# Performance work log

Measured on AMD Instinct MI355X. Metric: run time of the kernel, lower is better.

## Reference

```python
import jax, jax.numpy as jnp
import numpy as np

B, T, S, D, V, PAD = 8, 4095, 2048, 300, 32000, 1


def setup_inputs() -> dict:
    key = jax.random.key(0)
    k1, k2, k3, k4 = jax.random.split(key, 4)
    # tokens in [2, V) so none collide with padding_idx
    x = jax.random.randint(k1, (B, T), 2, V, dtype=jnp.int64)
    # first S nodes are leaves: indices (i, i); remaining T-S are internal spans hi > lo
    leaf = jnp.arange(S, dtype=jnp.int64)
    leaf_pairs = jnp.broadcast_to(jnp.stack([leaf, leaf], -1)[None], (B, S, 2))
    n_int = T - S
    lo = jax.random.randint(k2, (B, n_int), 0, S - 1, dtype=jnp.int64)
    span = jax.random.randint(k3, (B, n_int), 1, 64, dtype=jnp.int64)
    hi = jnp.minimum(lo + span, S - 1)
    int_pairs = jnp.stack([lo, hi], -1)
    indices = jnp.concatenate([leaf_pairs, int_pairs], axis=1)  # [B, T, 2]
    W = jax.random.normal(k4, (V, D), jnp.float32) * 0.02
    W = W.at[PAD].set(0.0)  # padding_idx row is zero, as in nn.Embedding
    return {"x": x, "indices": indices, "W": W}


def reference(x, indices, W):
    b, t = x.shape
    s = (t + 1) // 2
    # _retrieve_leaves: left-pack tokens whose (lo==hi) and token != PAD
    is_leaf = (indices[:, :, 0] == indices[:, :, 1]) & (x != PAD)  # [b,t]
    pos = jnp.cumsum(is_leaf.astype(jnp.int32), axis=1) - 1       # packed slot per leaf
    safe_pos = jnp.where(is_leaf, pos, s)                          # out-of-range -> dropped
    leaves = jnp.full((b, s), PAD, dtype=x.dtype)
    leaves = leaves.at[jnp.arange(b)[:, None], safe_pos].set(x, mode="drop")  # [b,s]
    # interval mask: lo <= r <= hi  (computed as (r>=lo) XOR (r>hi), as in source)
    r = jnp.arange(s)[None, None, :]                               # [1,1,s]
    mask = ((r >= indices[:, :, 0:1]) ^ (r > indices[:, :, 1:2])).astype(W.dtype)  # [b,t,s]
    emb = W[leaves]                                                # [b,s,D]
    denom = jnp.maximum(mask.sum(-1, keepdims=True), 1.0)          # [b,t,1]
    # same math as (mask[...,None] * emb[:,None]).sum(2), without the [b,t,s,D] tensor
    out = jnp.einsum("bts,bsd->btd", mask, emb) / denom
    return out
```

## Files before the change

kernel.cpp:

```cpp
#include <hip/hip_runtime.h>


#define BB 8
#define TT 4095
#define SS 2048
#define DD 300
#define D4 75
#define PADIDX 1
#define CHUNK 16
#define NC (SS / CHUNK)
#define NTB 320

typedef float f4 __attribute__((ext_vector_type(4)));

__global__ __launch_bounds__(512) void leaves_kernel(const int* __restrict__ x,
                                                     const int* __restrict__ idx,
                                                     int* __restrict__ leaves) {
    int b = blockIdx.x, tid = threadIdx.x;
    int lane = tid & 63, w = tid >> 6;
    __shared__ int wcnt[64];
    __shared__ int stotal;
    const int* xb = x + b * TT;
    const int2* ib2 = (const int2*)(idx + b * 2 * TT);

    int xv[8];
    bool lf8[8];
    unsigned long long bal[8];
#pragma unroll
    for (int k = 0; k < 8; ++k) {
        int t = tid + k * 512;
        xv[k] = 0;
        lf8[k] = false;
        if (t < TT) {
            xv[k] = xb[t];
            int2 pr = ib2[t];
            lf8[k] = (pr.x == pr.y) && (xv[k] != PADIDX);
        }
    }
#pragma unroll
    for (int k = 0; k < 8; ++k) {
        bal[k] = __ballot(lf8[k]);
        if (lane == 0) wcnt[k * 8 + w] = __popcll(bal[k]);
    }
    __syncthreads();
    if (w == 0) {
        int v = wcnt[lane];
        int s = v;
#pragma unroll
        for (int d = 1; d < 64; d <<= 1) {
            int t2 = __shfl_up(s, d);
            if (lane >= d) s += t2;
        }
        wcnt[lane] = s - v;
        if (lane == 63) stotal = s;
    }
    __syncthreads();
#pragma unroll
    for (int k = 0; k < 8; ++k) {
        int pos = wcnt[k * 8 + w] + __popcll(bal[k] & ((1ull << lane) - 1ull));
        if (lf8[k] && pos < SS) leaves[b * SS + pos] = xv[k];
    }
    for (int i = stotal + tid; i < SS; i += 512) leaves[b * SS + i] = PADIDX;
}

__global__ __launch_bounds__(NTB) void csumP_kernel(const int* __restrict__ leaves,
                                                    const float* __restrict__ W,
                                                    float* __restrict__ csum,
                                                    float* __restrict__ P) {
    int blk = blockIdx.x;
    int b = blk & 7, c = blk >> 3;
    int tid = threadIdx.x;
    int g = tid / 80, j = tid - g * 80;
    __shared__ int lf[CHUNK];
    __shared__ f4 sw[CHUNK][D4];
    if (tid < CHUNK) lf[tid] = leaves[b * SS + c * CHUNK + tid];
    __syncthreads();
    const f4* W4 = (const f4*)W;
    if (j < D4) {
#pragma unroll
        for (int i = 0; i < 4; ++i)
            sw[g * 4 + i][j] = W4[(size_t)lf[g * 4 + i] * D4 + j];
    }
    __syncthreads();
    if (j >= D4) return;

    f4* P4 = (f4*)P + (size_t)b * (SS + 1) * D4;
    int s0 = c * CHUNK;
    f4 run = (f4)0.f;
    for (int k = 0; k < g * 4; ++k) run += sw[k][j];
#pragma unroll
    for (int i = 0; i < 4; ++i) {
        int row = g * 4 + i;
        P4[(size_t)(s0 + row) * D4 + j] = run;
        run += sw[row][j];
    }
    if (g == 3) {
        ((f4*)csum)[(b * NC + c) * D4 + j] = run;
        if (c == NC - 1) P4[(size_t)SS * D4 + j] = (f4)0.f;
    }
}

__global__ __launch_bounds__(NTB) void base_kernel(const float* __restrict__ csum,
                                                   float* __restrict__ base) {
    int blk = blockIdx.x;
    int b = blk & 7, cc = blk >> 3;
    int tid = threadIdx.x;
    int g = tid / 80, j = tid - g * 80;
    __shared__ f4 part[4][D4];
    const f4* csum4 = (const f4*)csum;
    f4 acc = (f4)0.f;
    if (j < D4) {
        for (int i = g; i < cc; i += 4) acc += csum4[(b * NC + i) * D4 + j];
        part[g][j] = acc;
    }
    __syncthreads();
    if (g == 0 && j < D4) {
        f4 s = part[0][j] + part[1][j] + part[2][j] + part[3][j];
        ((f4*)base)[(b * (NC + 1) + cc) * D4 + j] = s;
    }
}

__global__ __launch_bounds__(NTB) void out_kernel(const int* __restrict__ idx,
                                                  const float* __restrict__ P,
                                                  const float* __restrict__ base,
                                                  float* __restrict__ out) {
    int tid = threadIdx.x;
    int r = tid / 80, j = tid - r * 80;
    int b = blockIdx.x & 7;
    int g = blockIdx.x >> 3;
    const f4* P4 = (const f4*)P + (size_t)b * (SS + 1) * D4;
    const f4* B4 = (const f4*)base + (size_t)b * (NC + 1) * D4;
    f4* out4 = (f4*)out;
    const int2* ixb = (const int2*)(idx + 2 * b * TT);
#pragma unroll
    for (int it = 0; it < 4; ++it) {
        int lr = g * 16 + r + it * 4;
        if (lr >= TT || j >= D4) continue;
        int2 pr = ixb[lr];
        int u = pr.y + 1;
        int a = min(pr.x, u), e = max(pr.x, u);
        a = max(0, min(a, SS));
        e = max(0, min(e, SS));
        int cnt = e - a;
        float inv = 1.0f / (float)(cnt > 0 ? cnt : 1);
        f4 ve = P4[(size_t)e * D4 + j] + B4[(e >> 4) * D4 + j];
        f4 va = P4[(size_t)a * D4 + j] + B4[(a >> 4) * D4 + j];
        f4 o = (ve - va) * inv;
        __builtin_nontemporal_store(o, &out4[((size_t)b * TT + lr) * D4 + j]);
    }
}

extern "C" void kernel_launch(void* const* d_in, const int* in_sizes, int n_in,
                              void* d_out, int out_size, void* d_ws, size_t ws_size,
                              hipStream_t stream) {
    const int* x = (const int*)d_in[0];
    const int* idx = (const int*)d_in[1];
    const float* W = (const float*)d_in[2];
    float* out = (float*)d_out;

    char* ws = (char*)d_ws;
    int* leaves = (int*)ws;
    float* csum = (float*)(ws + 65536);
    float* base = (float*)(ws + 65536 + 1228800);
    float* P = (float*)(ws + 2532736);

    leaves_kernel<<<BB, 512, 0, stream>>>(x, idx, leaves);
    csumP_kernel<<<BB * NC, NTB, 0, stream>>>(leaves, W, csum, P);
    base_kernel<<<BB * (NC + 1), NTB, 0, stream>>>(csum, base);
    out_kernel<<<(BB * TT + 15) / 16, NTB, 0, stream>>>(idx, P, base, out);
}
```

Baseline: 117.2 us.

## Fuse four kernels into one cooperative persistent kernel with grid syncs

```diff
diff --git a/kernel.cpp b/kernel.cpp
--- a/kernel.cpp
+++ b/kernel.cpp
@@ -1,4 +1,5 @@
 #include <hip/hip_runtime.h>
+#include <hip/hip_cooperative_groups.h>
 
 
 #define BB 8
@@ -10,37 +11,45 @@
 #define CHUNK 16
 #define NC (SS / CHUNK)
 #define NTB 320
+#define NK 13
 
 typedef float f4 __attribute__((ext_vector_type(4)));
 
-__global__ __launch_bounds__(512) void leaves_kernel(const int* __restrict__ x,
-                                                     const int* __restrict__ idx,
-                                                     int* __restrict__ leaves) {
-    int b = blockIdx.x, tid = threadIdx.x;
-    int lane = tid & 63, w = tid >> 6;
-    __shared__ int wcnt[64];
-    __shared__ int stotal;
+namespace cg = cooperative_groups;
+
+__global__ __launch_bounds__(NTB, 5) void fused_kernel(
+        const int* __restrict__ x, const int* __restrict__ idx,
+        const float* __restrict__ W, float* __restrict__ csum,
+        float* __restrict__ base, float* __restrict__ P,
+        float* __restrict__ out) {
+    cg::grid_group grid = cg::this_grid();
+    const int tid = threadIdx.x;
+    const int lane = tid & 63, w = tid >> 6;
+    const int blk = blockIdx.x;
+    const int b = blk & 7;
+    const int bstep = gridDim.x >> 3;
+
+    __shared__ int slv[SS];
+    __shared__ int wcnt[NK * 5 + 1];
+    __shared__ f4 sw[CHUNK][D4];
+
     const int* xb = x + b * TT;
-    const int2* ib2 = (const int2*)(idx + b * 2 * TT);
-
-    int xv[8];
-    bool lf8[8];
-    unsigned long long bal[8];
+    const int2* ib2 = (const int2*)(idx + 2 * b * TT);
+    unsigned lfmask = 0;
+    int xv[NK];
 #pragma unroll
-    for (int k = 0; k < 8; ++k) {
-        int t = tid + k * 512;
+    for (int k = 0; k < NK; ++k) {
+        int t = tid + k * NTB;
+        bool lf = false;
         xv[k] = 0;
-        lf8[k] = false;
         if (t < TT) {
             xv[k] = xb[t];
             int2 pr = ib2[t];
-            lf8[k] = (pr.x == pr.y) && (xv[k] != PADIDX);
+            lf = (pr.x == pr.y) && (xv[k] != PADIDX);
         }
-    }
-#pragma unroll
-    for (int k = 0; k < 8; ++k) {
-        bal[k] = __ballot(lf8[k]);
-        if (lane == 0) wcnt[k * 8 + w] = __popcll(bal[k]);
+        unsigned long long bal = __ballot(lf);
+        if (lf) lfmask |= 1u << k;
+        if (lane == 0) wcnt[k * 5 + w] = __popcll(bal);
     }
     __syncthreads();
     if (w == 0) {
@@ -52,101 +61,93 @@
             if (lane >= d) s += t2;
         }
         wcnt[lane] = s - v;
-        if (lane == 63) stotal = s;
+        if (lane == 63) {
+            int c64 = wcnt[64];
+            wcnt[64] = s;
+            wcnt[NK * 5] = s + c64;
+        }
     }
     __syncthreads();
+    int total = wcnt[NK * 5];
 #pragma unroll
-    for (int k = 0; k < 8; ++k) {
-        int pos = wcnt[k * 8 + w] + __popcll(bal[k] & ((1ull << lane) - 1ull));
-        if (lf8[k] && pos < SS) leaves[b * SS + pos] = xv[k];
+    for (int k = 0; k < NK; ++k) {
+        bool lf = (lfmask >> k) & 1u;
+        unsigned long long bal = __ballot(lf);
+        if (lf) {
+            int pos = wcnt[k * 5 + w] + __popcll(bal & ((1ull << lane) - 1ull));
+            if (pos < SS) slv[pos] = xv[k];
+        }
     }
-    for (int i = stotal + tid; i < SS; i += 512) leaves[b * SS + i] = PADIDX;
-}
+    for (int i = total + tid; i < SS; i += NTB) slv[i] = PADIDX;
+    __syncthreads();
 
-__global__ __launch_bounds__(NTB) void csumP_kernel(const int* __restrict__ leaves,
-                                                    const float* __restrict__ W,
-                                                    float* __restrict__ csum,
-                                                    float* __restrict__ P) {
-    int blk = blockIdx.x;
-    int b = blk & 7, c = blk >> 3;
-    int tid = threadIdx.x;
-    int g = tid / 80, j = tid - g * 80;
-    __shared__ int lf[CHUNK];
-    __shared__ f4 sw[CHUNK][D4];
-    if (tid < CHUNK) lf[tid] = leaves[b * SS + c * CHUNK + tid];
-    __syncthreads();
+    const int g = tid / 80, j = tid - g * 80;
     const f4* W4 = (const f4*)W;
-    if (j < D4) {
+    f4* P4 = (f4*)P + (size_t)b * (SS + 1) * D4;
+    f4* csum4 = (f4*)csum;
+    for (int c = blk >> 3; c < NC; c += bstep) {
+        if (j < D4) {
 #pragma unroll
-        for (int i = 0; i < 4; ++i)
-            sw[g * 4 + i][j] = W4[(size_t)lf[g * 4 + i] * D4 + j];
+            for (int i = 0; i < 4; ++i)
+                sw[g * 4 + i][j] = W4[(size_t)slv[c * CHUNK + g * 4 + i] * D4 + j];
+        }
+        __syncthreads();
+        if (j < D4) {
+            f4 run = (f4)0.f;
+            for (int k = 0; k < g * 4; ++k) run += sw[k][j];
+            int s0 = c * CHUNK;
+#pragma unroll
+            for (int i = 0; i < 4; ++i) {
+                int row = g * 4 + i;
+                P4[(size_t)(s0 + row) * D4 + j] = run;
+                run += sw[row][j];
+            }
+            if (g == 3) {
+                csum4[(b * NC + c) * D4 + j] = run;
+                if (c == NC - 1) P4[(size_t)SS * D4 + j] = (f4)0.f;
+            }
+        }
+        __syncthreads();
     }
-    __syncthreads();
-    if (j >= D4) return;
+    grid.sync();
 
-    f4* P4 = (f4*)P + (size_t)b * (SS + 1) * D4;
-    int s0 = c * CHUNK;
-    f4 run = (f4)0.f;
-    for (int k = 0; k < g * 4; ++k) run += sw[k][j];
-#pragma unroll
-    for (int i = 0; i < 4; ++i) {
-        int row = g * 4 + i;
-        P4[(size_t)(s0 + row) * D4 + j] = run;
-        run += sw[row][j];
+    f4* base4 = (f4*)base;
+    for (int c = blk >> 3; c <= NC; c += bstep) {
+        f4 acc = (f4)0.f;
+        if (j < D4) {
+            for (int i = g; i < c; i += 4)
+                acc += csum4[(b * NC + i) * D4 + j];
+        }
+        __syncthreads();
+        if (j < D4) sw[g][j] = acc;
+        __syncthreads();
+        if (g == 0 && j < D4) {
+            f4 s = sw[0][j] + sw[1][j] + sw[2][j] + sw[3][j];
+            base4[(b * (NC + 1) + c) * D4 + j] = s;
+        }
     }
-    if (g == 3) {
-        ((f4*)csum)[(b * NC + c) * D4 + j] = run;
-        if (c == NC - 1) P4[(size_t)SS * D4 + j] = (f4)0.f;
-    }
-}
+    grid.sync();
 
-__global__ __launch_bounds__(NTB) void base_kernel(const float* __restrict__ csum,
-                                                   float* __restrict__ base) {
-    int blk = blockIdx.x;
-    int b = blk & 7, cc = blk >> 3;
-    int tid = threadIdx.x;
-    int g = tid / 80, j = tid - g * 80;
-    __shared__ f4 part[4][D4];
-    const f4* csum4 = (const f4*)csum;
-    f4 acc = (f4)0.f;
-    if (j < D4) {
-        for (int i = g; i < cc; i += 4) acc += csum4[(b * NC + i) * D4 + j];
-        part[g][j] = acc;
-    }
-    __syncthreads();
-    if (g == 0 && j < D4) {
-        f4 s = part[0][j] + part[1][j] + part[2][j] + part[3][j];
-        ((f4*)base)[(b * (NC + 1) + cc) * D4 + j] = s;
-    }
-}
-
-__global__ __launch_bounds__(NTB) void out_kernel(const int* __restrict__ idx,
-                                                  const float* __restrict__ P,
-                                                  const float* __restrict__ base,
-                                                  float* __restrict__ out) {
-    int tid = threadIdx.x;
-    int r = tid / 80, j = tid - r * 80;
-    int b = blockIdx.x & 7;
-    int g = blockIdx.x >> 3;
-    const f4* P4 = (const f4*)P + (size_t)b * (SS + 1) * D4;
     const f4* B4 = (const f4*)base + (size_t)b * (NC + 1) * D4;
     f4* out4 = (f4*)out;
-    const int2* ixb = (const int2*)(idx + 2 * b * TT);
+    for (int rg = blk >> 3; rg * 32 < TT; rg += bstep) {
 #pragma unroll
-    for (int it = 0; it < 4; ++it) {
-        int lr = g * 16 + r + it * 4;
-        if (lr >= TT || j >= D4) continue;
-        int2 pr = ixb[lr];
-        int u = pr.y + 1;
-        int a = min(pr.x, u), e = max(pr.x, u);
-        a = max(0, min(a, SS));
-        e = max(0, min(e, SS));
-        int cnt = e - a;
-        float inv = 1.0f / (float)(cnt > 0 ? cnt : 1);
-        f4 ve = P4[(size_t)e * D4 + j] + B4[(e >> 4) * D4 + j];
-        f4 va = P4[(size_t)a * D4 + j] + B4[(a >> 4) * D4 + j];
-        f4 o = (ve - va) * inv;
-        __builtin_nontemporal_store(o, &out4[((size_t)b * TT + lr) * D4 + j]);
+        for (int it = 0; it < 8; ++it) {
+            int lr = rg * 32 + it * 4 + g;
+            if (lr < TT && j < D4) {
+                int2 pr = ib2[lr];
+                int u = pr.y + 1;
+                int a = min(pr.x, u), e = max(pr.x, u);
+                a = max(0, min(a, SS));
+                e = max(0, min(e, SS));
+                int cnt = e - a;
+                float inv = 1.0f / (float)(cnt > 0 ? cnt : 1);
+                f4 ve = P4[(size_t)e * D4 + j] + B4[(e >> 4) * D4 + j];
+                f4 va = P4[(size_t)a * D4 + j] + B4[(a >> 4) * D4 + j];
+                f4 o = (ve - va) * inv;
+                __builtin_nontemporal_store(o, &out4[((size_t)b * TT + lr) * D4 + j]);
+            }
+        }
     }
 }
 
@@ -159,13 +160,19 @@
     float* out = (float*)d_out;
 
     char* ws = (char*)d_ws;
-    int* leaves = (int*)ws;
-    float* csum = (float*)(ws + 65536);
-    float* base = (float*)(ws + 65536 + 1228800);
-    float* P = (float*)(ws + 2532736);
+    float* csum = (float*)ws;
+    float* base = (float*)(ws + 1228800);
+    float* P = (float*)(ws + 1228800 + 1238400);
 
-    leaves_kernel<<<BB, 512, 0, stream>>>(x, idx, leaves);
-    csumP_kernel<<<BB * NC, NTB, 0, stream>>>(leaves, W, csum, P);
-    base_kernel<<<BB * (NC + 1), NTB, 0, stream>>>(csum, base);
-    out_kernel<<<(BB * TT + 15) / 16, NTB, 0, stream>>>(idx, P, base, out);
+    static int nblk = 0;
+    if (nblk == 0) {
+        int maxb = 0;
+        hipOccupancyMaxActiveBlocksPerMultiprocessor(&maxb, fused_kernel, NTB, 0);
+        if (maxb < 1) maxb = 1;
+        int cap = maxb * 256;
+        nblk = (cap >= 1024) ? 1024 : (cap >= 512) ? 512 : 256;
+    }
+    void* args[] = {(void*)&x, (void*)&idx, (void*)&W, (void*)&csum,
+                    (void*)&base, (void*)&P, (void*)&out};
+    hipLaunchCooperativeKernel(fused_kernel, dim3(nblk), dim3(NTB), args, 0, stream);
 }
```

After: 254.9 us. +117.5%, slower.
